# Performance work log

Measured on AMD Instinct MI355X. Metric: run time of the kernel, lower is better.

Reference implementation:

```python
import jax, jax.numpy as jnp
import numpy as np

F = 128      # n_features
H = 512      # size_hidden
NT = 1       # n_targets
B = 512      # batch
T = 512      # seq_len


def setup_inputs() -> dict:
    key = jax.random.key(0)
    ks = jax.random.split(key, 7)
    s_ih = 1.0 / np.sqrt(H)
    return {
        "X": jax.random.normal(ks[0], (B, T, F), dtype=jnp.float32),
        # LSTMCell params (torch layout: [4H, in], gate order i, f, g, o)
        "W_ih": jax.random.uniform(ks[1], (4 * H, F), jnp.float32, -s_ih, s_ih),
        "W_hh": jax.random.uniform(ks[2], (4 * H, H), jnp.float32, -s_ih, s_ih),
        "b_ih": jax.random.uniform(ks[3], (4 * H,), jnp.float32, -s_ih, s_ih),
        "b_hh": jax.random.uniform(ks[4], (4 * H,), jnp.float32, -s_ih, s_ih),
        # final linear: size_hidden -> n_targets
        "W_out": jax.random.uniform(ks[5], (NT, H), jnp.float32, -s_ih, s_ih),
        "b_out": jax.random.uniform(ks[6], (NT,), jnp.float32, -s_ih, s_ih),
    }


def reference(X, W_ih, W_hh, b_ih, b_hh, W_out, b_out):
    Bsz = X.shape[0]
    Hd = W_hh.shape[1]

    # precompute input-to-gate projection for all timesteps: [B, T, 4H]
    x_gates = jnp.einsum('btf,gf->btg', X, W_ih) + b_ih + b_hh

    def step(carry, xg_t):
        h, c = carry
        gates = xg_t + h @ W_hh.T                      # [B, 4H]
        i, f, g, o = jnp.split(gates, 4, axis=-1)
        i = jax.nn.sigmoid(i)
        f = jax.nn.sigmoid(f)
        g = jnp.tanh(g)
        o = jax.nn.sigmoid(o)
        c = f * c + i * g
        h = o * jnp.tanh(c)
        out_t = h @ W_out.T + b_out                    # [B, NT]
        return (h, c), out_t

    h0 = jnp.zeros((Bsz, Hd), dtype=X.dtype)
    c0 = jnp.zeros((Bsz, Hd), dtype=X.dtype)
    xg = jnp.swapaxes(x_gates, 0, 1)                   # [T, B, 4H]
    _, outs = jax.lax.scan(step, (h0, c0), xg)         # [T, B, NT]
    return jnp.swapaxes(outs, 0, 1)                    # [B, T, NT]
```

## Files before the change

### kernel.cpp

```cpp
#include <hip/hip_runtime.h>

#define Hd   512
#define Fd   128
#define Td   512
#define Bd   512
#define TG   64
#define BG   64
#define WPG  32
#define LDH  520
#define LDG  68

typedef __bf16 bf16x8 __attribute__((ext_vector_type(8)));
typedef float  f32x4  __attribute__((ext_vector_type(4)));
typedef unsigned int u32x4 __attribute__((ext_vector_type(4)));
typedef unsigned int u32x2 __attribute__((ext_vector_type(2)));

__device__ __forceinline__ unsigned short f2bf(float x) {
    unsigned u = __float_as_uint(x);
    unsigned r = (u + 0x7fffu + ((u >> 16) & 1u)) >> 16;
    return (unsigned short)r;
}
__device__ __forceinline__ float sigm(float x) {
    return 1.0f / (1.0f + __expf(-x));
}
__device__ __forceinline__ float tanh_fast(float x) {
    float xc = fminf(fmaxf(x, -15.f), 15.f);
    float e  = __expf(2.f * xc);
    return (e - 1.f) / (e + 1.f);
}
__device__ __forceinline__ bf16x8 pack8(const float* p) {
    float4 a = *(const float4*)p;
    float4 b = *(const float4*)(p + 4);
    union { unsigned short u[8]; bf16x8 v; } r;
    r.u[0] = f2bf(a.x); r.u[1] = f2bf(a.y); r.u[2] = f2bf(a.z); r.u[3] = f2bf(a.w);
    r.u[4] = f2bf(b.x); r.u[5] = f2bf(b.y); r.u[6] = f2bf(b.z); r.u[7] = f2bf(b.w);
    return r.v;
}

__global__ __launch_bounds__(256, 1) void lstm_persist(
    const float* __restrict__ X,     const float* __restrict__ W_ih,
    const float* __restrict__ W_hh,  const float* __restrict__ b_ih,
    const float* __restrict__ b_hh,  const float* __restrict__ W_out,
    const float* __restrict__ b_out, float* __restrict__ out,
    unsigned short* __restrict__ hbuf,
    unsigned int*  __restrict__ bar)
{
    extern __shared__ char smem[];
    unsigned short* htile = (unsigned short*)smem;
    float*          gsum  = (float*)smem;
    float*          biasl = (float*)(smem + TG * LDH * 2);
    float*          hpart = biasl + TG;

    const int tid = threadIdx.x;
    const int gid = blockIdx.x;
    const int grp = gid & 7;
    const int r   = gid >> 3;
    const int bb  = grp * BG;
    const int jb  = r * 16;

    const int lane = tid & 63, wid = tid >> 6;
    const int m16  = lane & 15, quad = lane >> 4;
    const int gr0  = (wid & 1) * 32;
    const int bt0  = (wid >> 1) * 32;
    const int brow0 = bb + bt0 + m16;
    const int brow1 = brow0 + 16;
    const unsigned short* hl0 = htile + (bt0 + m16) * LDH + quad * 8;
    const unsigned short* hl1 = hl0 + 16 * LDH;

    bf16x8 wh0[16], wh1[16], wx0[4], wx1[4];
    {
        const int lr0 = gr0 + m16, lr1 = lr0 + 16;
        const int gw0 = ((lr0 >> 4) * Hd) + jb + (lr0 & 15);
        const int gw1 = ((lr1 >> 4) * Hd) + jb + (lr1 & 15);
        const float* ph0 = W_hh + (size_t)gw0 * Hd + quad * 8;
        const float* ph1 = W_hh + (size_t)gw1 * Hd + quad * 8;
        const float* px0 = W_ih + (size_t)gw0 * Fd + quad * 8;
        const float* px1 = W_ih + (size_t)gw1 * Fd + quad * 8;
#pragma unroll
        for (int ks = 0; ks < 16; ++ks) {
            wh0[ks] = pack8(ph0 + ks * 32);
            wh1[ks] = pack8(ph1 + ks * 32);
        }
#pragma unroll
        for (int ks = 0; ks < 4; ++ks) {
            wx0[ks] = pack8(px0 + ks * 32);
            wx1[ks] = pack8(px1 + ks * 32);
        }
    }
    if (tid < TG) {
        int grow = ((tid >> 4) * Hd) + jb + (tid & 15);
        biasl[tid] = b_ih[grow] + b_hh[grow];
    }
    __syncthreads();

    const int eb  = tid & 63;
    const int jjb = (tid >> 6) << 2;
    float wout[4];
#pragma unroll
    for (int u = 0; u < 4; ++u) wout[u] = W_out[jb + jjb + u];
    const float bo = b_out[0];
    float cst[4] = {0.f, 0.f, 0.f, 0.f};

    unsigned int* mybar = bar + grp * 32;
    unsigned short* hw_lds = htile + (size_t)(tid >> 6) * LDH + (tid & 63) * 8;

    f32x4 acc00, acc01, acc10, acc11;
    const float* xp0 = X + (size_t)brow0 * (Td * Fd) + quad * 8;
    const float* xp1 = X + (size_t)brow1 * (Td * Fd) + quad * 8;

    auto do_xpart = [&]() {
#pragma unroll
        for (int ks = 0; ks < 4; ++ks) {
            float4 xa = *(const float4*)(xp0 + ks * 32);
            float4 xb = *(const float4*)(xp0 + ks * 32 + 4);
            float4 ya = *(const float4*)(xp1 + ks * 32);
            float4 yb = *(const float4*)(xp1 + ks * 32 + 4);
            bf16x8 b0, b1;
            b0[0]=(__bf16)xa.x; b0[1]=(__bf16)xa.y; b0[2]=(__bf16)xa.z; b0[3]=(__bf16)xa.w;
            b0[4]=(__bf16)xb.x; b0[5]=(__bf16)xb.y; b0[6]=(__bf16)xb.z; b0[7]=(__bf16)xb.w;
            b1[0]=(__bf16)ya.x; b1[1]=(__bf16)ya.y; b1[2]=(__bf16)ya.z; b1[3]=(__bf16)ya.w;
            b1[4]=(__bf16)yb.x; b1[5]=(__bf16)yb.y; b1[6]=(__bf16)yb.z; b1[7]=(__bf16)yb.w;
            acc00 = __builtin_amdgcn_mfma_f32_16x16x32_bf16(wx0[ks], b0, acc00, 0, 0, 0);
            acc01 = __builtin_amdgcn_mfma_f32_16x16x32_bf16(wx0[ks], b1, acc01, 0, 0, 0);
            acc10 = __builtin_amdgcn_mfma_f32_16x16x32_bf16(wx1[ks], b0, acc10, 0, 0, 0);
            acc11 = __builtin_amdgcn_mfma_f32_16x16x32_bf16(wx1[ks], b1, acc11, 0, 0, 0);
        }
    };

    acc00 = f32x4{0.f,0.f,0.f,0.f}; acc01 = f32x4{0.f,0.f,0.f,0.f};
    acc10 = f32x4{0.f,0.f,0.f,0.f}; acc11 = f32x4{0.f,0.f,0.f,0.f};
    do_xpart();

    for (int t = 0; t < Td; ++t) {
        if (t > 0 && tid == 0) {
            unsigned tgt = (unsigned)t * WPG;
            while (__hip_atomic_load(mybar, __ATOMIC_RELAXED, __HIP_MEMORY_SCOPE_AGENT) < tgt)
                __builtin_amdgcn_s_sleep(2);
        }
        __syncthreads();

        const unsigned short* hprev = hbuf + (size_t)((t & 1) ^ 1) * (Bd * Hd);

        u32x4 hv0,hv1,hv2,hv3,hv4,hv5,hv6,hv7,hv8,hv9,hv10,hv11,hv12,hv13,hv14,hv15;
        {
            const unsigned short* p0 =
                hprev + (size_t)(bb + (tid >> 6)) * Hd + (tid & 63) * 8;
            const unsigned short* b0p = p0 + 1 * 2048;
            const unsigned short* b1p = p0 + 3 * 2048;
            const unsigned short* b2p = p0 + 5 * 2048;
            const unsigned short* b3p = p0 + 7 * 2048;
            const unsigned short* b4p = p0 + 9 * 2048;
            const unsigned short* b5p = p0 + 11 * 2048;
            const unsigned short* b6p = p0 + 13 * 2048;
            const unsigned short* b7p = p0 + 15 * 2048;
            asm volatile(
                "global_load_dwordx4 %0,  %16, off offset:-4096 sc1\n\t"
                "global_load_dwordx4 %1,  %16, off sc1\n\t"
                "global_load_dwordx4 %2,  %17, off offset:-4096 sc1\n\t"
                "global_load_dwordx4 %3,  %17, off sc1\n\t"
                "global_load_dwordx4 %4,  %18, off offset:-4096 sc1\n\t"
                "global_load_dwordx4 %5,  %18, off sc1\n\t"
                "global_load_dwordx4 %6,  %19, off offset:-4096 sc1\n\t"
                "global_load_dwordx4 %7,  %19, off sc1\n\t"
                "global_load_dwordx4 %8,  %20, off offset:-4096 sc1\n\t"
                "global_load_dwordx4 %9,  %20, off sc1\n\t"
                "global_load_dwordx4 %10, %21, off offset:-4096 sc1\n\t"
                "global_load_dwordx4 %11, %21, off sc1\n\t"
                "global_load_dwordx4 %12, %22, off offset:-4096 sc1\n\t"
                "global_load_dwordx4 %13, %22, off sc1\n\t"
                "global_load_dwordx4 %14, %23, off offset:-4096 sc1\n\t"
                "global_load_dwordx4 %15, %23, off sc1\n\t"
                "s_waitcnt vmcnt(0)"
                : "=&v"(hv0), "=&v"(hv1), "=&v"(hv2), "=&v"(hv3),
                  "=&v"(hv4), "=&v"(hv5), "=&v"(hv6), "=&v"(hv7),
                  "=&v"(hv8), "=&v"(hv9), "=&v"(hv10), "=&v"(hv11),
                  "=&v"(hv12), "=&v"(hv13), "=&v"(hv14), "=&v"(hv15)
                : "v"(b0p), "v"(b1p), "v"(b2p), "v"(b3p),
                  "v"(b4p), "v"(b5p), "v"(b6p), "v"(b7p)
                : "memory");
        }
        *(u32x4*)(hw_lds + 0 * 2080)  = hv0;  *(u32x4*)(hw_lds + 1 * 2080)  = hv1;
        *(u32x4*)(hw_lds + 2 * 2080)  = hv2;  *(u32x4*)(hw_lds + 3 * 2080)  = hv3;
        *(u32x4*)(hw_lds + 4 * 2080)  = hv4;  *(u32x4*)(hw_lds + 5 * 2080)  = hv5;
        *(u32x4*)(hw_lds + 6 * 2080)  = hv6;  *(u32x4*)(hw_lds + 7 * 2080)  = hv7;
        *(u32x4*)(hw_lds + 8 * 2080)  = hv8;  *(u32x4*)(hw_lds + 9 * 2080)  = hv9;
        *(u32x4*)(hw_lds + 10 * 2080) = hv10; *(u32x4*)(hw_lds + 11 * 2080) = hv11;
        *(u32x4*)(hw_lds + 12 * 2080) = hv12; *(u32x4*)(hw_lds + 13 * 2080) = hv13;
        *(u32x4*)(hw_lds + 14 * 2080) = hv14; *(u32x4*)(hw_lds + 15 * 2080) = hv15;
        __syncthreads();

#pragma unroll
        for (int ks = 0; ks < 16; ++ks) {
            bf16x8 b0 = *(const bf16x8*)(hl0 + ks * 32);
            bf16x8 b1 = *(const bf16x8*)(hl1 + ks * 32);
            acc00 = __builtin_amdgcn_mfma_f32_16x16x32_bf16(wh0[ks], b0, acc00, 0, 0, 0);
            acc01 = __builtin_amdgcn_mfma_f32_16x16x32_bf16(wh0[ks], b1, acc01, 0, 0, 0);
            acc10 = __builtin_amdgcn_mfma_f32_16x16x32_bf16(wh1[ks], b0, acc10, 0, 0, 0);
            acc11 = __builtin_amdgcn_mfma_f32_16x16x32_bf16(wh1[ks], b1, acc11, 0, 0, 0);
        }
        __syncthreads();

        {
            const int row = gr0 + (quad << 2);
            const int col = bt0 + m16;
            float* g00 = gsum + row * LDG + col;
            float* g10 = gsum + (row + 16) * LDG + col;
#pragma unroll
            for (int v = 0; v < 4; ++v) {
                g00[v * LDG]      = acc00[v];
                g00[v * LDG + 16] = acc01[v];
                g10[v * LDG]      = acc10[v];
                g10[v * LDG + 16] = acc11[v];
            }
        }
        __syncthreads();

        float part = 0.f;
        unsigned short hvb[4];
#pragma unroll
        for (int u = 0; u < 4; ++u) {
            int jj = jjb + u;
            float pi = gsum[jj * LDG + eb]        + biasl[jj];
            float pf = gsum[(16 + jj) * LDG + eb] + biasl[16 + jj];
            float pg = gsum[(32 + jj) * LDG + eb] + biasl[32 + jj];
            float po = gsum[(48 + jj) * LDG + eb] + biasl[48 + jj];
            float ii = sigm(pi), ff = sigm(pf);
            float gg = tanh_fast(pg), oo = sigm(po);
            float c  = ff * cst[u] + ii * gg;
            cst[u]   = c;
            float h  = oo * tanh_fast(c);
            hvb[u]   = f2bf(h);
            part    += h * wout[u];
        }
        {
            u32x2 hd2;
            hd2[0] = (unsigned)hvb[0] | ((unsigned)hvb[1] << 16);
            hd2[1] = (unsigned)hvb[2] | ((unsigned)hvb[3] << 16);
            unsigned short* hwp =
                hbuf + (size_t)(t & 1) * (Bd * Hd) + (size_t)(bb + eb) * Hd + jb + jjb;
            asm volatile("global_store_dwordx2 %0, %1, off sc1"
                         :: "v"(hwp), "v"(hd2) : "memory");
            asm volatile("s_waitcnt vmcnt(0)" ::: "memory");
        }
        if (tid == 0)
            __hip_atomic_fetch_add(mybar, 1u, __ATOMIC_RELAXED, __HIP_MEMORY_SCOPE_AGENT);

        hpart[tid] = part;

        acc00 = f32x4{0.f,0.f,0.f,0.f}; acc01 = f32x4{0.f,0.f,0.f,0.f};
        acc10 = f32x4{0.f,0.f,0.f,0.f}; acc11 = f32x4{0.f,0.f,0.f,0.f};
        if (t + 1 < Td) {
            xp0 += Fd; xp1 += Fd;
            do_xpart();
        }

        __syncthreads();
        if (tid < 64) {
            float s = hpart[tid] + hpart[tid + 64] + hpart[tid + 128] + hpart[tid + 192];
            if (r == 0) s += bo;
            atomicAdd(out + (size_t)(bb + tid) * Td + t, s);
        }
    }
}

extern "C" void kernel_launch(void* const* d_in, const int* in_sizes, int n_in,
                              void* d_out, int out_size, void* d_ws, size_t ws_size,
                              hipStream_t stream) {
    const float* X     = (const float*)d_in[0];
    const float* W_ih  = (const float*)d_in[1];
    const float* W_hh  = (const float*)d_in[2];
    const float* b_ih  = (const float*)d_in[3];
    const float* b_hh  = (const float*)d_in[4];
    const float* W_out = (const float*)d_in[5];
    const float* b_out = (const float*)d_in[6];
    float* out = (float*)d_out;

    unsigned short* hbuf = (unsigned short*)d_ws;
    unsigned int*   bar  = (unsigned int*)((char*)d_ws + 2u * Bd * Hd * 2u);

    hipMemsetAsync(d_ws, 0, 2u * Bd * Hd * 2u + 4096u, stream);
    hipMemsetAsync(d_out, 0, (size_t)out_size * sizeof(float), stream);

    const size_t smem = (size_t)TG * LDH * 2
                      + TG * 4 + 256 * 4;
    (void)hipFuncSetAttribute((const void*)lstm_persist,
                              hipFuncAttributeMaxDynamicSharedMemorySize, (int)smem);

    lstm_persist<<<dim3(256), dim3(256), smem, stream>>>(
        X, W_ih, W_hh, b_ih, b_hh, W_out, b_out, out, hbuf, bar);
}
```

Before: 3.922 ms.

## Use XCD-local cache scope for barrier and h exchange when groups share an XCD

At startup each block records its hardware XCC id, and all blocks meet at a one-time rendezvous to check whether every block in its 32-block sync group sits on the same XCD. If they do, the per-step barrier polling, the h-state loads and stores, and the barrier atomic use narrower cache-scope bits (sc0 or none) instead of sc1, so traffic can stay in the XCD-local L2 rather than going to device-coherent memory. Otherwise the original path runs. The gain depends on how the hardware places blocks on XCDs. The new spin loop has no sleep and so polls more aggressively, and the startup check adds a global rendezvous plus extra reserved barrier memory.

```diff
diff --git a/kernel.cpp b/kernel.cpp
--- a/kernel.cpp
+++ b/kernel.cpp
@@ -36,6 +36,33 @@
     r.u[4] = f2bf(b.x); r.u[5] = f2bf(b.y); r.u[6] = f2bf(b.z); r.u[7] = f2bf(b.w);
     return r.v;
 }
+
+#define HLOAD_BLOCK(SC)                                                     \
+    asm volatile(                                                           \
+        "global_load_dwordx4 %0,  %16, off offset:-4096 " SC "\n\t"         \
+        "global_load_dwordx4 %1,  %16, off " SC "\n\t"                      \
+        "global_load_dwordx4 %2,  %17, off offset:-4096 " SC "\n\t"         \
+        "global_load_dwordx4 %3,  %17, off " SC "\n\t"                      \
+        "global_load_dwordx4 %4,  %18, off offset:-4096 " SC "\n\t"         \
+        "global_load_dwordx4 %5,  %18, off " SC "\n\t"                      \
+        "global_load_dwordx4 %6,  %19, off offset:-4096 " SC "\n\t"         \
+        "global_load_dwordx4 %7,  %19, off " SC "\n\t"                      \
+        "global_load_dwordx4 %8,  %20, off offset:-4096 " SC "\n\t"         \
+        "global_load_dwordx4 %9,  %20, off " SC "\n\t"                      \
+        "global_load_dwordx4 %10, %21, off offset:-4096 " SC "\n\t"         \
+        "global_load_dwordx4 %11, %21, off " SC "\n\t"                      \
+        "global_load_dwordx4 %12, %22, off offset:-4096 " SC "\n\t"         \
+        "global_load_dwordx4 %13, %22, off " SC "\n\t"                      \
+        "global_load_dwordx4 %14, %23, off offset:-4096 " SC "\n\t"         \
+        "global_load_dwordx4 %15, %23, off " SC "\n\t"                      \
+        "s_waitcnt vmcnt(0)"                                                \
+        : "=&v"(hv0), "=&v"(hv1), "=&v"(hv2), "=&v"(hv3),                   \
+          "=&v"(hv4), "=&v"(hv5), "=&v"(hv6), "=&v"(hv7),                   \
+          "=&v"(hv8), "=&v"(hv9), "=&v"(hv10), "=&v"(hv11),                 \
+          "=&v"(hv12), "=&v"(hv13), "=&v"(hv14), "=&v"(hv15)                \
+        : "v"(b0p), "v"(b1p), "v"(b2p), "v"(b3p),                           \
+          "v"(b4p), "v"(b5p), "v"(b6p), "v"(b7p)                            \
+        : "memory")
 
 __global__ __launch_bounds__(256, 1) void lstm_persist(
     const float* __restrict__ X,     const float* __restrict__ W_ih,
@@ -91,7 +118,28 @@
         int grow = ((tid >> 4) * Hd) + jb + (tid & 15);
         biasl[tid] = b_ih[grow] + b_hh[grow];
     }
+
+    unsigned myxcd;
+    asm volatile("s_getreg_b32 %0, hwreg(HW_REG_XCC_ID)" : "=s"(myxcd));
+    if (tid == 0) {
+        unsigned int* xcdid = bar + 256;
+        unsigned int* ready = bar + 240;
+        asm volatile("global_store_dword %0, %1, off sc1\n\ts_waitcnt vmcnt(0)"
+                     :: "v"(xcdid + gid), "v"(myxcd) : "memory");
+        __hip_atomic_fetch_add(ready, 1u, __ATOMIC_RELAXED, __HIP_MEMORY_SCOPE_AGENT);
+        while (__hip_atomic_load(ready, __ATOMIC_RELAXED, __HIP_MEMORY_SCOPE_AGENT) < 256u)
+            __builtin_amdgcn_s_sleep(4);
+        unsigned ok = 1;
+        for (int j = 0; j < WPG; ++j) {
+            unsigned v;
+            asm volatile("global_load_dword %0, %1, off sc1\n\ts_waitcnt vmcnt(0)"
+                         : "=v"(v) : "v"(xcdid + (grp + 8 * j)) : "memory");
+            ok &= (v == myxcd) ? 1u : 0u;
+        }
+        ((unsigned*)hpart)[0] = ok;
+    }
     __syncthreads();
+    const bool fast = ((const unsigned*)hpart)[0] != 0;
 
     const int eb  = tid & 63;
     const int jjb = (tid >> 6) << 2;
@@ -134,8 +182,18 @@
     for (int t = 0; t < Td; ++t) {
         if (t > 0 && tid == 0) {
             unsigned tgt = (unsigned)t * WPG;
-            while (__hip_atomic_load(mybar, __ATOMIC_RELAXED, __HIP_MEMORY_SCOPE_AGENT) < tgt)
-                __builtin_amdgcn_s_sleep(2);
+            if (fast) {
+                for (;;) {
+                    unsigned v;
+                    asm volatile("global_load_dword %0, %1, off sc0\n\t"
+                                 "s_waitcnt vmcnt(0)"
+                                 : "=v"(v) : "v"(mybar) : "memory");
+                    if (v >= tgt) break;
+                }
+            } else {
+                while (__hip_atomic_load(mybar, __ATOMIC_RELAXED, __HIP_MEMORY_SCOPE_AGENT) < tgt)
+                    __builtin_amdgcn_s_sleep(2);
+            }
         }
         __syncthreads();
 
@@ -153,31 +211,7 @@
             const unsigned short* b5p = p0 + 11 * 2048;
             const unsigned short* b6p = p0 + 13 * 2048;
             const unsigned short* b7p = p0 + 15 * 2048;
-            asm volatile(
-                "global_load_dwordx4 %0,  %16, off offset:-4096 sc1\n\t"
-                "global_load_dwordx4 %1,  %16, off sc1\n\t"
-                "global_load_dwordx4 %2,  %17, off offset:-4096 sc1\n\t"
-                "global_load_dwordx4 %3,  %17, off sc1\n\t"
-                "global_load_dwordx4 %4,  %18, off offset:-4096 sc1\n\t"
-                "global_load_dwordx4 %5,  %18, off sc1\n\t"
-                "global_load_dwordx4 %6,  %19, off offset:-4096 sc1\n\t"
-                "global_load_dwordx4 %7,  %19, off sc1\n\t"
-                "global_load_dwordx4 %8,  %20, off offset:-4096 sc1\n\t"
-                "global_load_dwordx4 %9,  %20, off sc1\n\t"
-                "global_load_dwordx4 %10, %21, off offset:-4096 sc1\n\t"
-                "global_load_dwordx4 %11, %21, off sc1\n\t"
-                "global_load_dwordx4 %12, %22, off offset:-4096 sc1\n\t"
-                "global_load_dwordx4 %13, %22, off sc1\n\t"
-                "global_load_dwordx4 %14, %23, off offset:-4096 sc1\n\t"
-                "global_load_dwordx4 %15, %23, off sc1\n\t"
-                "s_waitcnt vmcnt(0)"
-                : "=&v"(hv0), "=&v"(hv1), "=&v"(hv2), "=&v"(hv3),
-                  "=&v"(hv4), "=&v"(hv5), "=&v"(hv6), "=&v"(hv7),
-                  "=&v"(hv8), "=&v"(hv9), "=&v"(hv10), "=&v"(hv11),
-                  "=&v"(hv12), "=&v"(hv13), "=&v"(hv14), "=&v"(hv15)
-                : "v"(b0p), "v"(b1p), "v"(b2p), "v"(b3p),
-                  "v"(b4p), "v"(b5p), "v"(b6p), "v"(b7p)
-                : "memory");
+            if (fast) { HLOAD_BLOCK("sc0"); } else { HLOAD_BLOCK("sc1"); }
         }
         *(u32x4*)(hw_lds + 0 * 2080)  = hv0;  *(u32x4*)(hw_lds + 1 * 2080)  = hv1;
         *(u32x4*)(hw_lds + 2 * 2080)  = hv2;  *(u32x4*)(hw_lds + 3 * 2080)  = hv3;
@@ -238,12 +272,24 @@
             hd2[1] = (unsigned)hvb[2] | ((unsigned)hvb[3] << 16);
             unsigned short* hwp =
                 hbuf + (size_t)(t & 1) * (Bd * Hd) + (size_t)(bb + eb) * Hd + jb + jjb;
-            asm volatile("global_store_dwordx2 %0, %1, off sc1"
-                         :: "v"(hwp), "v"(hd2) : "memory");
+            if (fast) {
+                asm volatile("global_store_dwordx2 %0, %1, off"
+                             :: "v"(hwp), "v"(hd2) : "memory");
+            } else {
+                asm volatile("global_store_dwordx2 %0, %1, off sc1"
+                             :: "v"(hwp), "v"(hd2) : "memory");
+            }
             asm volatile("s_waitcnt vmcnt(0)" ::: "memory");
         }
-        if (tid == 0)
-            __hip_atomic_fetch_add(mybar, 1u, __ATOMIC_RELAXED, __HIP_MEMORY_SCOPE_AGENT);
+        if (tid == 0) {
+            if (fast) {
+                unsigned one = 1u;
+                asm volatile("global_atomic_add %0, %1, off"
+                             :: "v"(mybar), "v"(one) : "memory");
+            } else {
+                __hip_atomic_fetch_add(mybar, 1u, __ATOMIC_RELAXED, __HIP_MEMORY_SCOPE_AGENT);
+            }
+        }
 
         hpart[tid] = part;
 
```

Measured after the change: 3.425 ms. 1.15x faster.
